# Kernel optimization log

Hardware: AMD Instinct MI355X
Metric: run time of the kernel (lower is better)

Reference implementation:

```python
import jax, jax.numpy as jnp
import numpy as np

B, S, HID = 2, 2048, 1024
NH = 16
HD = HID // NH  # 64


def rope_cos_sin(seq_len, dim, dtype=jnp.float32):
    inv_freq = 1.0 / (10000.0 ** (jnp.arange(0, dim, 2, dtype=jnp.float32) / dim))
    t = jnp.arange(seq_len, dtype=jnp.float32)
    freqs = jnp.outer(t, inv_freq)            # [S, dim/2]
    emb = jnp.concatenate([freqs, freqs], -1)  # [S, dim]
    return jnp.cos(emb).astype(dtype), jnp.sin(emb).astype(dtype)


def rotate_half(x):
    x1, x2 = jnp.split(x, 2, axis=-1)
    return jnp.concatenate([-x2, x1], axis=-1)


def apply_rope(x, cos, sin):
    # x: [B, H, S, D]; cos/sin: [S, D]
    return x * cos[None, None] + rotate_half(x) * sin[None, None]


def setup_inputs() -> dict:
    key = jax.random.key(0)
    ks = jax.random.split(key, 7)
    scale = 0.02
    return {
        "hidden_states": jax.random.normal(ks[0], (B, S, HID), jnp.float32),
        "attention_mask": jnp.zeros((B, 1, 1, S), jnp.float32),
        "Wq": jax.random.normal(ks[1], (HID, HID), jnp.float32) * scale,
        "bq": jnp.zeros((HID,), jnp.float32),
        "Wk": jax.random.normal(ks[2], (HID, HID), jnp.float32) * scale,
        "bk": jnp.zeros((HID,), jnp.float32),
        "Wv": jax.random.normal(ks[3], (HID, HID), jnp.float32) * scale,
        "bv": jnp.zeros((HID,), jnp.float32),
    }


def reference(hidden_states, attention_mask, Wq, bq, Wk, bk, Wv, bv):
    def split_heads(x):  # [B,S,HID] -> [B,H,S,D]
        return x.reshape(B, S, NH, HD).transpose(0, 2, 1, 3)

    q = split_heads(hidden_states @ Wq + bq)
    k = split_heads(hidden_states @ Wk + bk)
    v = split_heads(hidden_states @ Wv + bv)

    q = q * (HD ** -0.5)
    cos, sin = rope_cos_sin(S, HD, q.dtype)
    q = apply_rope(q, cos, sin)
    k = apply_rope(k, cos, sin)

    scores = jnp.einsum("bhqd,bhkd->bhqk", q, k) + attention_mask
    probs = jax.nn.softmax(scores, axis=-1)
    ctx = jnp.einsum("bhqk,bhkd->bhqd", probs, v)
    ctx = ctx.transpose(0, 2, 1, 3).reshape(B, S, HID)
    return ctx
```

## Files before the change

### kernel.cpp

```cpp
#include <hip/hip_runtime.h>
#include <math.h>

namespace {
constexpr int B_ = 2, S_ = 2048, HID_ = 1024, NH_ = 16, HD_ = 64;
constexpr int M_ = B_ * S_;
constexpr int QSZ = B_ * NH_ * S_ * HD_;
constexpr int TBL = S_ * (HD_ / 2);
constexpr float LOG2E = 1.4426950408889634f;

typedef float f32x4 __attribute__((ext_vector_type(4)));
typedef __bf16 bf16x8 __attribute__((ext_vector_type(8)));
typedef unsigned int u32x4 __attribute__((ext_vector_type(4)));
typedef unsigned short u16;

__device__ inline u16 f2bf(float x) {
  unsigned int u = __float_as_uint(x);
  return (u16)((u + 0x7fffu + ((u >> 16) & 1u)) >> 16);
}
__device__ inline float bf2f(u16 h) {
  return __uint_as_float(((unsigned int)h) << 16);
}

typedef __attribute__((address_space(1))) const unsigned int as1_u32;
typedef __attribute__((address_space(3))) unsigned int as3_u32;
__device__ __forceinline__ void gll16(const void* g, void* l) {
  __builtin_amdgcn_global_load_lds((as1_u32*)g, (as3_u32*)l, 16, 0, 0);
}

__device__ __forceinline__ void swap32(unsigned int& a, unsigned int& b) {
  asm("v_permlane32_swap_b32 %0, %1" : "+v"(a), "+v"(b));
}
__device__ __forceinline__ void swap16(unsigned int& a, unsigned int& b) {
  asm("v_permlane16_swap_b32 %0, %1" : "+v"(a), "+v"(b));
}
__device__ __forceinline__ unsigned int cvtpk(float lo, float hi) {
  unsigned int r;
  asm("v_cvt_pk_bf16_f32 %0, %1, %2" : "=v"(r) : "v"(lo), "v"(hi));
  return r;
}

__global__ void rope_table_kernel(float* __restrict__ ct, float* __restrict__ st) {
  int t = blockIdx.x * blockDim.x + threadIdx.x;
  if (t >= TBL) return;
  int s = t >> 5, i = t & 31;
  float inv = 1.0f / powf(10000.0f, (float)(2 * i) / (float)HD_);
  float ang = (float)s * inv;
  double a = (double)ang;
  ct[t] = (float)cos(a);
  st[t] = (float)sin(a);
}

__global__ __launch_bounds__(256)
void convert_hs_kernel(const float* __restrict__ hs, u16* __restrict__ hh) {
  size_t t = (size_t)blockIdx.x * 256 + threadIdx.x;
  float4 v = *(const float4*)&hs[t * 4];
  short4 hi = {(short)f2bf(v.x), (short)f2bf(v.y), (short)f2bf(v.z), (short)f2bf(v.w)};
  *(short4*)&hh[t * 4] = hi;
}

__global__ __launch_bounds__(256)
void transpose_w_kernel(const float* __restrict__ Wq, const float* __restrict__ Wk,
                        const float* __restrict__ Wv, u16* __restrict__ wt) {
  __shared__ float tile[64][65];
  const float* W = blockIdx.z == 0 ? Wq : blockIdx.z == 1 ? Wk : Wv;
  int k0 = blockIdx.x * 64, n0 = blockIdx.y * 64;
  int t = threadIdx.x;
  int lrow = t >> 4, lcol = (t & 15) * 4;
#pragma unroll
  for (int i = 0; i < 4; ++i) {
    float4 v = *(const float4*)&W[(size_t)(k0 + lrow + i * 16) * HID_ + n0 + lcol];
    tile[lrow + i * 16][lcol + 0] = v.x;
    tile[lrow + i * 16][lcol + 1] = v.y;
    tile[lrow + i * 16][lcol + 2] = v.z;
    tile[lrow + i * 16][lcol + 3] = v.w;
  }
  __syncthreads();
  int n = t >> 2, ks = (t & 3) * 16;
  u16 tmp[16];
#pragma unroll
  for (int j = 0; j < 16; ++j) tmp[j] = f2bf(tile[ks + j][n]);
  u16* dst = &wt[((size_t)blockIdx.z * 1024 + n0 + n) * 1024 + k0 + ks];
  ((uint4*)dst)[0] = ((uint4*)tmp)[0];
  ((uint4*)dst)[1] = ((uint4*)tmp)[1];
}

__global__ __launch_bounds__(256)
void proj_gemm_kernel(const u16* __restrict__ Ah, const u16* __restrict__ Wt,
                      const float* __restrict__ bq, const float* __restrict__ bk,
                      const float* __restrict__ bv,
                      const float* __restrict__ ct, const float* __restrict__ st,
                      u16* __restrict__ qw, u16* __restrict__ kw, u16* __restrict__ vt) {
  __shared__ u16 sAh[128 * 64];
  __shared__ u16 sB[128 * 64];
  const int tid = threadIdx.x;
  const int wave = tid >> 6, lane = tid & 63;
  const int lr = lane & 15, lg = lane >> 4;

  int bid = blockIdx.x;
  int swz = (bid & 7) * 96 + (bid >> 3);
  const int gx = swz / 24, gy = swz % 24;
  const int m0 = gx * 128;
  const int ng0 = gy * 128;

  size_t aoff[4], boff[4];
  int c16[4];
#pragma unroll
  for (int i = 0; i < 4; ++i) {
    int c = i * 256 + tid;
    int row = c >> 3, ks = c & 7;
    int kph = (ks ^ (row & 7)) * 8;
    aoff[i] = (size_t)(m0 + row) * HID_ + kph;
    boff[i] = (size_t)(ng0 + row) * HID_ + kph;
    c16[i] = c * 16;
  }

  const int wr = (wave >> 1) * 64, wc = (wave & 1) * 64;
  int offA[4][2], offB[4][2];
#pragma unroll
  for (int f = 0; f < 4; ++f) {
    int ra = wr + f * 16 + lr;
    int rb = wc + f * 16 + lr;
#pragma unroll
    for (int kk = 0; kk < 2; ++kk) {
      offA[f][kk] = ra * 128 + (((kk * 4 + lg)) ^ (ra & 7)) * 16;
      offB[f][kk] = rb * 128 + (((kk * 4 + lg)) ^ (rb & 7)) * 16;
    }
  }

  f32x4 acc[4][4];
#pragma unroll
  for (int mf = 0; mf < 4; ++mf)
#pragma unroll
    for (int nf = 0; nf < 4; ++nf) acc[mf][nf] = (f32x4){0.f, 0.f, 0.f, 0.f};

  for (int k0 = 0; k0 < HID_; k0 += 64) {
    __syncthreads();
#pragma unroll
    for (int i = 0; i < 4; ++i) {
      gll16(Ah + aoff[i] + k0, (char*)sAh + c16[i]);
      gll16(Wt + boff[i] + k0, (char*)sB + c16[i]);
    }
    __syncthreads();
#pragma unroll
    for (int kk = 0; kk < 2; ++kk) {
      bf16x8 a_h[4], bb[4];
#pragma unroll
      for (int f = 0; f < 4; ++f) {
        a_h[f] = *(const bf16x8*)((const char*)sAh + offA[f][kk]);
        bb[f] = *(const bf16x8*)((const char*)sB + offB[f][kk]);
      }
      __builtin_amdgcn_s_setprio(1);
#pragma unroll
      for (int mf = 0; mf < 4; ++mf)
#pragma unroll
        for (int nf = 0; nf < 4; ++nf)
          acc[mf][nf] = __builtin_amdgcn_mfma_f32_16x16x32_bf16(a_h[mf], bb[nf], acc[mf][nf], 0, 0, 0);
      __builtin_amdgcn_s_setprio(0);
    }
  }

  const int which = gy >> 3;
  const int colm = (gy & 7) * 128 + wc;
  const int h = colm >> 6;
  const float* bias = which == 0 ? bq : which == 1 ? bk : bv;
  const float scale = which == 0 ? 0.125f * LOG2E : 1.0f;

  if (which < 2) {
    u16* oh = which == 0 ? qw : kw;
#pragma unroll
    for (int mf = 0; mf < 4; ++mf) {
#pragma unroll
      for (int r = 0; r < 4; ++r) {
        int m = m0 + wr + mf * 16 + lg * 4 + r;
        int b = m >> 11, s = m & (S_ - 1);
        size_t rowb = (((size_t)b * NH_ + h) * S_ + s) * HD_;
#pragma unroll
        for (int nf = 0; nf < 2; ++nf) {
          int d = nf * 16 + lr;
          float x1 = acc[mf][nf][r] + bias[colm + d];
          float x2 = acc[mf][nf + 2][r] + bias[colm + d + 32];
          float cth = ct[s * 32 + d], sth = st[s * 32 + d];
          oh[rowb + d]      = f2bf((x1 * cth - x2 * sth) * scale);
          oh[rowb + d + 32] = f2bf((x2 * cth + x1 * sth) * scale);
        }
      }
    }
  } else {
#pragma unroll
    for (int mf = 0; mf < 4; ++mf) {
      int mB = m0 + wr + mf * 16 + lg * 4;
      int b = mB >> 11, s0 = mB & (S_ - 1);
#pragma unroll
      for (int nf = 0; nf < 4; ++nf) {
        int d = nf * 16 + lr;
        float bi = bias[colm + d];
        ushort4 pk;
        pk.x = f2bf(acc[mf][nf][0] + bi);
        pk.y = f2bf(acc[mf][nf][1] + bi);
        pk.z = f2bf(acc[mf][nf][2] + bi);
        pk.w = f2bf(acc[mf][nf][3] + bi);
        *(ushort4*)&vt[(((size_t)b * NH_ + h) * HD_ + d) * S_ + s0] = pk;
      }
    }
  }
}

__global__ __launch_bounds__(256, 2)
void attn_mfma_kernel(const u16* __restrict__ qw, const u16* __restrict__ kw,
                      const u16* __restrict__ vt, const float* __restrict__ mask,
                      float* __restrict__ outp) {
  __shared__ __align__(16) char smem[40960];
  constexpr int VTB = 16384, MS = 32768;
  const int tid = threadIdx.x;
  const int wave = tid >> 6, lane = tid & 63;
  const int lr = lane & 15, lg = lane >> 4;

  const int bid = blockIdx.x;
  const int idx = bid >> 3;
  const int bh = (bid & 7) * 4 + (idx >> 4);
  const int q0 = (idx & 15) * 128;
  const int b = bh >> 4, h = bh & 15;
  const size_t hb = (size_t)bh * S_ * HD_;

  {
    const float* mrow = mask + (size_t)b * S_ + tid * 8;
    float4 v0 = *(const float4*)mrow;
    float4 v1 = *(const float4*)(mrow + 4);
    v0.x *= LOG2E; v0.y *= LOG2E; v0.z *= LOG2E; v0.w *= LOG2E;
    v1.x *= LOG2E; v1.y *= LOG2E; v1.z *= LOG2E; v1.w *= LOG2E;
    *(float4*)(smem + MS + tid * 32) = v0;
    *(float4*)(smem + MS + tid * 32 + 16) = v1;
  }

  bf16x8 aq[2][2];
#pragma unroll
  for (int qb = 0; qb < 2; ++qb) {
    size_t base = hb + (size_t)(q0 + wave * 32 + qb * 16 + lr) * HD_ + lg * 8;
    aq[qb][0] = *(const bf16x8*)&qw[base];
    aq[qb][1] = *(const bf16x8*)&qw[base + 32];
  }

  bf16x8 ones_f;
  {
    unsigned int w = (lr == 0) ? 0x3F803F80u : 0u;
    u32x4 f = {w, w, w, w};
    ones_f = *(bf16x8*)&f;
  }

  f32x4 O[2][4], O4[2];
  float mrun[2];
#pragma unroll
  for (int qb = 0; qb < 2; ++qb) {
    mrun[qb] = -INFINITY;
    O4[qb] = (f32x4){0.f, 0.f, 0.f, 0.f};
#pragma unroll
    for (int dt = 0; dt < 4; ++dt) O[qb][dt] = (f32x4){0.f, 0.f, 0.f, 0.f};
  }

  size_t kgo[4], vgo[4];
  int klo_[4], vlo_[4];
#pragma unroll
  for (int i = 0; i < 4; ++i) {
    int a = i * 4096 + tid * 16;
    {
      int row = a >> 7, seg = (a >> 4) & 7;
      kgo[i] = (size_t)row * HD_ + ((seg ^ (row & 7)) * 8);
      klo_[i] = a;
    }
    {
      int row = a >> 8, seg = (a >> 4) & 15;
      int sg = (seg & 8) | ((seg & 7) ^ (row & 7));
      vgo[i] = (size_t)row * S_ + sg * 8;
      vlo_[i] = VTB + a;
    }
  }

  const int sw = (lr & 7) << 4;

  for (int k0 = 0; k0 < S_; k0 += 128) {
    __syncthreads();
#pragma unroll
    for (int i = 0; i < 4; ++i) {
      gll16(kw + hb + kgo[i] + (size_t)k0 * HD_, smem + klo_[i]);
      gll16(vt + hb + vgo[i] + k0, smem + vlo_[i]);
    }
    __syncthreads();

    f32x4 sc[2][8];
#pragma unroll
    for (int qb = 0; qb < 2; ++qb)
#pragma unroll
      for (int c = 0; c < 8; ++c) sc[qb][c] = (f32x4){0.f, 0.f, 0.f, 0.f};
    __builtin_amdgcn_s_setprio(1);
#pragma unroll
    for (int t2 = 0; t2 < 2; ++t2) {
#pragma unroll
      for (int c = 0; c < 8; ++c) {
        int off = ((c * 16 + lr) << 7) + ((t2 * 64 + lg * 16) ^ sw);
        bf16x8 kf = *(const bf16x8*)(smem + off);
        sc[0][c] = __builtin_amdgcn_mfma_f32_16x16x32_bf16(kf, aq[0][t2], sc[0][c], 0, 0, 0);
        sc[1][c] = __builtin_amdgcn_mfma_f32_16x16x32_bf16(kf, aq[1][t2], sc[1][c], 0, 0, 0);
      }
    }
    __builtin_amdgcn_s_setprio(0);

    f32x4 mk[8];
#pragma unroll
    for (int c = 0; c < 8; ++c)
      mk[c] = *(const f32x4*)(smem + MS + (k0 + c * 16 + lg * 4) * 4);

    bf16x8 pf[2][4];
#pragma unroll
    for (int qb = 0; qb < 2; ++qb) {
      float mx = -INFINITY;
#pragma unroll
      for (int c = 0; c < 8; ++c) {
        sc[qb][c] += mk[c];
#pragma unroll
        for (int r = 0; r < 4; ++r) mx = fmaxf(mx, sc[qb][c][r]);
      }
      mx = fmaxf(mx, __shfl_xor(mx, 16));
      mx = fmaxf(mx, __shfl_xor(mx, 32));
      if (mx > mrun[qb] + 8.f) {
        float corr = __builtin_amdgcn_exp2f(mrun[qb] - mx);
        mrun[qb] = mx;
        O4[qb] *= corr;
#pragma unroll
        for (int dt = 0; dt < 4; ++dt) O[qb][dt] *= corr;
      }
#pragma unroll
      for (int c = 0; c < 8; ++c)
#pragma unroll
        for (int r = 0; r < 4; ++r)
          sc[qb][c][r] = __builtin_amdgcn_exp2f(sc[qb][c][r] - mrun[qb]);

#pragma unroll
      for (int kt = 0; kt < 4; ++kt) {
        unsigned int x0 = cvtpk(sc[qb][2 * kt][0], sc[qb][2 * kt][1]);
        unsigned int x1 = cvtpk(sc[qb][2 * kt + 1][0], sc[qb][2 * kt + 1][1]);
        unsigned int y0 = cvtpk(sc[qb][2 * kt][2], sc[qb][2 * kt][3]);
        unsigned int y1 = cvtpk(sc[qb][2 * kt + 1][2], sc[qb][2 * kt + 1][3]);
        swap32(x0, x1);
        swap16(x0, x1);
        swap32(y0, y1);
        swap16(y0, y1);
        u32x4 f = {x0, y0, x1, y1};
        pf[qb][kt] = *(bf16x8*)&f;
      }
    }

    __builtin_amdgcn_s_setprio(1);
#pragma unroll
    for (int kt = 0; kt < 4; ++kt) {
      O4[0] = __builtin_amdgcn_mfma_f32_16x16x32_bf16(ones_f, pf[0][kt], O4[0], 0, 0, 0);
      O4[1] = __builtin_amdgcn_mfma_f32_16x16x32_bf16(ones_f, pf[1][kt], O4[1], 0, 0, 0);
#pragma unroll
      for (int dt = 0; dt < 4; ++dt) {
        int off = VTB + ((dt * 16 + lr) << 8) + ((kt * 64 + lg * 16) ^ sw);
        bf16x8 vf = *(const bf16x8*)(smem + off);
        O[0][dt] = __builtin_amdgcn_mfma_f32_16x16x32_bf16(vf, pf[0][kt], O[0][dt], 0, 0, 0);
        O[1][dt] = __builtin_amdgcn_mfma_f32_16x16x32_bf16(vf, pf[1][kt], O[1][dt], 0, 0, 0);
      }
    }
    __builtin_amdgcn_s_setprio(0);
  }

#pragma unroll
  for (int qb = 0; qb < 2; ++qb) {
    float l = __shfl(O4[qb][0], lr, 64);
    float inv = 1.0f / l;
    int s = q0 + wave * 32 + qb * 16 + lr;
    size_t rowb = ((size_t)b * S_ + s) * HID_ + h * HD_;
#pragma unroll
    for (int dt = 0; dt < 4; ++dt) {
      float4 r;
      r.x = O[qb][dt][0] * inv;
      r.y = O[qb][dt][1] * inv;
      r.z = O[qb][dt][2] * inv;
      r.w = O[qb][dt][3] * inv;
      *(float4*)&outp[rowb + dt * 16 + lg * 4] = r;
    }
  }
}

}

extern "C" void kernel_launch(void* const* d_in, const int* in_sizes, int n_in,
                              void* d_out, int out_size, void* d_ws, size_t ws_size,
                              hipStream_t stream) {
  const float* hs   = (const float*)d_in[0];
  const float* mask = (const float*)d_in[1];
  const float* Wq   = (const float*)d_in[2];
  const float* bq   = (const float*)d_in[3];
  const float* Wk   = (const float*)d_in[4];
  const float* bk   = (const float*)d_in[5];
  const float* Wv   = (const float*)d_in[6];
  const float* bv   = (const float*)d_in[7];

  u16* qw = (u16*)d_ws;
  u16* kw = qw + QSZ;
  u16* vt = kw + QSZ;
  u16* hh = vt + QSZ;
  u16* wt = hh + (size_t)M_ * HID_;
  float* ct = (float*)(wt + (size_t)3 * 1024 * 1024);
  float* st = ct + TBL;

  rope_table_kernel<<<TBL / 256, 256, 0, stream>>>(ct, st);
  convert_hs_kernel<<<(M_ * HID_) / 1024, 256, 0, stream>>>(hs, hh);
  transpose_w_kernel<<<dim3(16, 16, 3), 256, 0, stream>>>(Wq, Wk, Wv, wt);

  proj_gemm_kernel<<<768, 256, 0, stream>>>(hh, wt, bq, bk, bv, ct, st, qw, kw, vt);

  attn_mfma_kernel<<<512, 256, 0, stream>>>(qw, kw, vt, mask, (float*)d_out);
}
```

Before: 113.9 us.

## Double-buffer LDS tiles in projection GEMM and attention KV loop

The projection GEMM gets two LDS buffers per operand, so the next K-slice's global-to-LDS loads are issued before computing on the current slice, with partial vmcnt waits and raw barriers. The attention kernel halves its KV tile from 128 to 64 keys and ping-pongs two 16 KB buffers inside the existing 32 KB region, again overlapping the next tile's loads with the current tile's compute. This aims to hide global load latency that the old load-sync-compute pattern exposed. In exchange, the GEMM doubles its LDS footprint, which may reduce occupancy, and attention runs twice as many iterations and barriers.

```diff
diff --git a/kernel.cpp b/kernel.cpp
--- a/kernel.cpp
+++ b/kernel.cpp
@@ -90,8 +90,8 @@
                       const float* __restrict__ bv,
                       const float* __restrict__ ct, const float* __restrict__ st,
                       u16* __restrict__ qw, u16* __restrict__ kw, u16* __restrict__ vt) {
-  __shared__ u16 sAh[128 * 64];
-  __shared__ u16 sB[128 * 64];
+  __shared__ u16 sAh[2][128 * 64];
+  __shared__ u16 sB[2][128 * 64];
   const int tid = threadIdx.x;
   const int wave = tid >> 6, lane = tid & 63;
   const int lr = lane & 15, lg = lane >> 4;
@@ -133,21 +133,38 @@
 #pragma unroll
     for (int nf = 0; nf < 4; ++nf) acc[mf][nf] = (f32x4){0.f, 0.f, 0.f, 0.f};
 
-  for (int k0 = 0; k0 < HID_; k0 += 64) {
-    __syncthreads();
-#pragma unroll
-    for (int i = 0; i < 4; ++i) {
-      gll16(Ah + aoff[i] + k0, (char*)sAh + c16[i]);
-      gll16(Wt + boff[i] + k0, (char*)sB + c16[i]);
-    }
-    __syncthreads();
+#pragma unroll
+  for (int i = 0; i < 4; ++i) {
+    gll16(Ah + aoff[i], (char*)sAh[0] + c16[i]);
+    gll16(Wt + boff[i], (char*)sB[0] + c16[i]);
+  }
+  __syncthreads();
+
+  for (int t = 0; t < 16; ++t) {
+    if (t < 15) {
+      const int nb = (t + 1) & 1;
+      const int k0n = (t + 1) * 64;
+#pragma unroll
+      for (int i = 0; i < 4; ++i) {
+        gll16(Ah + aoff[i] + k0n, (char*)sAh[nb] + c16[i]);
+        gll16(Wt + boff[i] + k0n, (char*)sB[nb] + c16[i]);
+      }
+      asm volatile("s_waitcnt vmcnt(8)" ::: "memory");
+    } else {
+      asm volatile("s_waitcnt vmcnt(0)" ::: "memory");
+    }
+    __builtin_amdgcn_s_barrier();
+    __builtin_amdgcn_sched_barrier(0);
+
+    const char* sa = (const char*)sAh[t & 1];
+    const char* sb = (const char*)sB[t & 1];
 #pragma unroll
     for (int kk = 0; kk < 2; ++kk) {
       bf16x8 a_h[4], bb[4];
 #pragma unroll
       for (int f = 0; f < 4; ++f) {
-        a_h[f] = *(const bf16x8*)((const char*)sAh + offA[f][kk]);
-        bb[f] = *(const bf16x8*)((const char*)sB + offB[f][kk]);
+        a_h[f] = *(const bf16x8*)(sa + offA[f][kk]);
+        bb[f] = *(const bf16x8*)(sb + offB[f][kk]);
       }
       __builtin_amdgcn_s_setprio(1);
 #pragma unroll
@@ -157,6 +174,8 @@
           acc[mf][nf] = __builtin_amdgcn_mfma_f32_16x16x32_bf16(a_h[mf], bb[nf], acc[mf][nf], 0, 0, 0);
       __builtin_amdgcn_s_setprio(0);
     }
+    __builtin_amdgcn_sched_barrier(0);
+    __builtin_amdgcn_s_barrier();
   }
 
   const int which = gy >> 3;
@@ -210,7 +229,7 @@
                       const u16* __restrict__ vt, const float* __restrict__ mask,
                       float* __restrict__ outp) {
   __shared__ __align__(16) char smem[40960];
-  constexpr int VTB = 16384, MS = 32768;
+  constexpr int MS = 32768;
   const int tid = threadIdx.x;
   const int wave = tid >> 6, lane = tid & 63;
   const int lr = lane & 15, lg = lane >> 4;
@@ -257,46 +276,54 @@
     for (int dt = 0; dt < 4; ++dt) O[qb][dt] = (f32x4){0.f, 0.f, 0.f, 0.f};
   }
 
-  size_t kgo[4], vgo[4];
-  int klo_[4], vlo_[4];
-#pragma unroll
-  for (int i = 0; i < 4; ++i) {
+  size_t kgo[2], vgo[2];
+  int klo_[2], vlo_[2];
+#pragma unroll
+  for (int i = 0; i < 2; ++i) {
     int a = i * 4096 + tid * 16;
-    {
-      int row = a >> 7, seg = (a >> 4) & 7;
-      kgo[i] = (size_t)row * HD_ + ((seg ^ (row & 7)) * 8);
-      klo_[i] = a;
-    }
-    {
-      int row = a >> 8, seg = (a >> 4) & 15;
-      int sg = (seg & 8) | ((seg & 7) ^ (row & 7));
-      vgo[i] = (size_t)row * S_ + sg * 8;
-      vlo_[i] = VTB + a;
-    }
+    int row = a >> 7, seg = (a >> 4) & 7;
+    int sseg = (seg ^ (row & 7)) * 8;
+    kgo[i] = (size_t)row * HD_ + sseg;
+    klo_[i] = a;
+    vgo[i] = (size_t)row * S_ + sseg;
+    vlo_[i] = 8192 + a;
   }
 
   const int sw = (lr & 7) << 4;
 
-  for (int k0 = 0; k0 < S_; k0 += 128) {
-    __syncthreads();
-#pragma unroll
-    for (int i = 0; i < 4; ++i) {
-      gll16(kw + hb + kgo[i] + (size_t)k0 * HD_, smem + klo_[i]);
-      gll16(vt + hb + vgo[i] + k0, smem + vlo_[i]);
-    }
-    __syncthreads();
-
-    f32x4 sc[2][8];
+#define STAGE_KV(T, BASE)                                                   \
+  {                                                                         \
+    _Pragma("unroll") for (int i = 0; i < 2; ++i) {                         \
+      gll16(kw + hb + kgo[i] + (size_t)(T) * 64 * HD_, smem + (BASE) + klo_[i]); \
+      gll16(vt + hb + vgo[i] + (T) * 64, smem + (BASE) + vlo_[i]);          \
+    }                                                                       \
+  }
+
+  STAGE_KV(0, 0);
+  __syncthreads();
+
+  for (int t = 0; t < 32; ++t) {
+    const int base = (t & 1) << 14;
+    if (t < 31) {
+      STAGE_KV(t + 1, ((t + 1) & 1) << 14);
+      asm volatile("s_waitcnt vmcnt(4)" ::: "memory");
+    } else {
+      asm volatile("s_waitcnt vmcnt(0)" ::: "memory");
+    }
+    __builtin_amdgcn_s_barrier();
+    __builtin_amdgcn_sched_barrier(0);
+
+    f32x4 sc[2][4];
 #pragma unroll
     for (int qb = 0; qb < 2; ++qb)
 #pragma unroll
-      for (int c = 0; c < 8; ++c) sc[qb][c] = (f32x4){0.f, 0.f, 0.f, 0.f};
+      for (int c = 0; c < 4; ++c) sc[qb][c] = (f32x4){0.f, 0.f, 0.f, 0.f};
     __builtin_amdgcn_s_setprio(1);
 #pragma unroll
     for (int t2 = 0; t2 < 2; ++t2) {
 #pragma unroll
-      for (int c = 0; c < 8; ++c) {
-        int off = ((c * 16 + lr) << 7) + ((t2 * 64 + lg * 16) ^ sw);
+      for (int c = 0; c < 4; ++c) {
+        int off = base + ((c * 16 + lr) << 7) + ((t2 * 64 + lg * 16) ^ sw);
         bf16x8 kf = *(const bf16x8*)(smem + off);
         sc[0][c] = __builtin_amdgcn_mfma_f32_16x16x32_bf16(kf, aq[0][t2], sc[0][c], 0, 0, 0);
         sc[1][c] = __builtin_amdgcn_mfma_f32_16x16x32_bf16(kf, aq[1][t2], sc[1][c], 0, 0, 0);
@@ -304,17 +331,17 @@
     }
     __builtin_amdgcn_s_setprio(0);
 
-    f32x4 mk[8];
-#pragma unroll
-    for (int c = 0; c < 8; ++c)
-      mk[c] = *(const f32x4*)(smem + MS + (k0 + c * 16 + lg * 4) * 4);
-
-    bf16x8 pf[2][4];
+    f32x4 mk[4];
+#pragma unroll
+    for (int c = 0; c < 4; ++c)
+      mk[c] = *(const f32x4*)(smem + MS + (t * 64 + c * 16 + lg * 4) * 4);
+
+    bf16x8 pf[2][2];
 #pragma unroll
     for (int qb = 0; qb < 2; ++qb) {
       float mx = -INFINITY;
 #pragma unroll
-      for (int c = 0; c < 8; ++c) {
+      for (int c = 0; c < 4; ++c) {
         sc[qb][c] += mk[c];
 #pragma unroll
         for (int r = 0; r < 4; ++r) mx = fmaxf(mx, sc[qb][c][r]);
@@ -329,13 +356,13 @@
         for (int dt = 0; dt < 4; ++dt) O[qb][dt] *= corr;
       }
 #pragma unroll
-      for (int c = 0; c < 8; ++c)
+      for (int c = 0; c < 4; ++c)
 #pragma unroll
         for (int r = 0; r < 4; ++r)
           sc[qb][c][r] = __builtin_amdgcn_exp2f(sc[qb][c][r] - mrun[qb]);
 
 #pragma unroll
-      for (int kt = 0; kt < 4; ++kt) {
+      for (int kt = 0; kt < 2; ++kt) {
         unsigned int x0 = cvtpk(sc[qb][2 * kt][0], sc[qb][2 * kt][1]);
         unsigned int x1 = cvtpk(sc[qb][2 * kt + 1][0], sc[qb][2 * kt + 1][1]);
         unsigned int y0 = cvtpk(sc[qb][2 * kt][2], sc[qb][2 * kt][3]);
@@ -351,18 +378,21 @@
 
     __builtin_amdgcn_s_setprio(1);
 #pragma unroll
-    for (int kt = 0; kt < 4; ++kt) {
+    for (int kt = 0; kt < 2; ++kt) {
       O4[0] = __builtin_amdgcn_mfma_f32_16x16x32_bf16(ones_f, pf[0][kt], O4[0], 0, 0, 0);
       O4[1] = __builtin_amdgcn_mfma_f32_16x16x32_bf16(ones_f, pf[1][kt], O4[1], 0, 0, 0);
 #pragma unroll
       for (int dt = 0; dt < 4; ++dt) {
-        int off = VTB + ((dt * 16 + lr) << 8) + ((kt * 64 + lg * 16) ^ sw);
+        int off = base + 8192 + ((dt * 16 + lr) << 7) + ((kt * 64 + lg * 16) ^ sw);
         bf16x8 vf = *(const bf16x8*)(smem + off);
         O[0][dt] = __builtin_amdgcn_mfma_f32_16x16x32_bf16(vf, pf[0][kt], O[0][dt], 0, 0, 0);
         O[1][dt] = __builtin_amdgcn_mfma_f32_16x16x32_bf16(vf, pf[1][kt], O[1][dt], 0, 0, 0);
       }
     }
     __builtin_amdgcn_s_setprio(0);
+
+    __builtin_amdgcn_sched_barrier(0);
+    __builtin_amdgcn_s_barrier();
   }
 
 #pragma unroll
@@ -381,6 +411,7 @@
       *(float4*)&outp[rowb + dt * 16 + lg * 4] = r;
     }
   }
+#undef STAGE_KV
 }
 
 }
```

Measured after the change: 112.7 us. No clear change (-1.0%).
